# Kernel optimization log

Measured on AMD Instinct MI355X. Metric: run time of the kernel, lower is better.

Reference implementation:

```python
import jax, jax.numpy as jnp
import numpy as np

VEC_DIM = 32
RANK = 2
D = H = W = 40


def setup_inputs() -> dict:
    key = jax.random.key(0)
    k1, k2, k3 = jax.random.split(key, 3)
    volume = jax.random.normal(k1, (D, H, W, VEC_DIM), dtype=jnp.float32)
    # M is nn.Linear(m, m, bias=False) init uniform(-0.5, 0.5)
    M_weight = jax.random.uniform(k2, (VEC_DIM, VEC_DIM), jnp.float32, -0.5, 0.5)
    # P init uniform(-0.1, 0.1)
    P = jax.random.uniform(k3, (VEC_DIM, VEC_DIM), jnp.float32, -0.1, 0.1)
    return {"volume": volume, "M_weight": M_weight, "P": P}


def reference(volume, M_weight, P):
    m = volume.shape[-1]
    r = RANK
    # --- extract_windows: linear mode (step=1), rank_mode='drop', rank_op='avg' ---
    # mean over each r x r x r cubic window == sum-pool / r^3 (VALID padding = drop)
    pooled = jax.lax.reduce_window(
        volume, 0.0, jax.lax.add,
        window_dimensions=(r, r, r, 1),
        window_strides=(1, 1, 1, 1),
        padding="VALID",
    ) / float(r ** 3)  # [Dp, Hp, Wp, m]
    Dp, Hp, Wp = pooled.shape[:3]
    vecs = pooled.reshape(-1, m)  # [B, m], B = Dp*Hp*Wp (window order: k1 outer, k3 inner)
    k1 = jnp.arange(Dp, dtype=jnp.float32)
    k2 = jnp.arange(Hp, dtype=jnp.float32)
    k3 = jnp.arange(Wp, dtype=jnp.float32)
    k1g, k2g, k3g = jnp.meshgrid(k1, k2, k3, indexing="ij")
    k1f, k2f, k3f = k1g.ravel(), k2g.ravel(), k3g.ravel()  # [B]
    # --- batch_compute_Nk ---
    # periods[i, j] = i*m + j + 2
    periods = (jnp.arange(m, dtype=jnp.float32)[:, None] * m
               + jnp.arange(m, dtype=jnp.float32)[None, :] + 2.0)  # [m, m]
    two_pi = 2.0 * jnp.pi
    inv_p = two_pi / periods  # [m, m]
    # phi[b, i, j] = cos(2pi*k1/p) * cos(2pi*k2/p) * cos(2pi*k3/p)
    phi = (jnp.cos(k1f[:, None, None] * inv_p)
           * jnp.cos(k2f[:, None, None] * inv_p)
           * jnp.cos(k3f[:, None, None] * inv_p))  # [B, m, m]
    x = vecs @ M_weight.T  # nn.Linear: x = v W^T, [B, m]
    Nk = jnp.einsum("bj,ij,bij->bi", x, P, phi)  # [B, m]
    return Nk
```

## Files before the change

### kernel.cpp

```cpp
#include <hip/hip_runtime.h>
#include <math.h>

constexpr int DV = 40;
constexpr int NP = 39;
constexpr int VD = 32;
constexpr float TWO_PI = 6.28318530717958647692f;

__global__ __launch_bounds__(256) void ndk_kernel(
    const float* __restrict__ vol,
    const float* __restrict__ Mw,
    const float* __restrict__ P,
    float* __restrict__ out)
{
    __shared__ float  Mt[VD * VD];
    __shared__ float2 RI[VD * VD];
    __shared__ float  pool[8 * VD];
    __shared__ float  xs[NP * VD];

    const int tid = threadIdx.x;
    const int bx  = blockIdx.x;
    const int k1  = bx / NP;
    const int k2  = bx % NP;
    const float k1f = (float)k1, k2f = (float)k2;

    for (int t = tid; t < VD * VD; t += 256) {
        const int row = t >> 5;
        const int col = t & 31;
        Mt[col * VD + row] = Mw[t];
        const float w = TWO_PI / (float)(row * VD + col + 2);
        const float r = P[t] * __cosf(k1f * w) * __cosf(k2f * w);
        RI[col * VD + row] = make_float2(r, w);
    }
    __syncthreads();

    {
        const int c = tid & 31;
        const int s = tid >> 5;
        for (int chunk = 0; chunk < 5; ++chunk) {
            const int k3 = chunk * 8 + s;
            float pv = 0.f;
            if (k3 < NP) {
                const float* vp = vol + ((size_t)(k1 * DV + k2) * DV + k3) * VD + c;
                constexpr int SW = VD;
                constexpr int SH = DV * VD;
                constexpr int SD = DV * DV * VD;
                pv = vp[0]       + vp[SW]
                   + vp[SH]      + vp[SH + SW]
                   + vp[SD]      + vp[SD + SW]
                   + vp[SD + SH] + vp[SD + SH + SW];
                pv *= 0.125f;
            }
            pool[s * VD + c] = pv;
            __syncthreads();
            if (k3 < NP) {
                const int j = c;
                float x = 0.f;
                #pragma unroll
                for (int cc = 0; cc < VD; ++cc)
                    x += pool[s * VD + cc] * Mt[cc * VD + j];
                xs[k3 * VD + j] = x;
            }
            __syncthreads();
        }
    }

    {
        const int i   = tid & 31;
        const int sub = tid >> 5;
        const long bbase = (long)bx * NP;
        for (int k3 = sub; k3 < NP; k3 += 8) {
            const float k3f = (float)k3;
            float acc = 0.f;
            #pragma unroll
            for (int j = 0; j < VD; ++j) {
                const float2 ri = RI[j * VD + i];
                acc += xs[k3 * VD + j] * ri.x * __cosf(k3f * ri.y);
            }
            out[(bbase + k3) * VD + i] = acc;
        }
    }
}

extern "C" void kernel_launch(void* const* d_in, const int* in_sizes, int n_in,
                              void* d_out, int out_size, void* d_ws, size_t ws_size,
                              hipStream_t stream) {
    const float* vol = (const float*)d_in[0];
    const float* Mw  = (const float*)d_in[1];
    const float* P   = (const float*)d_in[2];
    float* out = (float*)d_out;
    (void)in_sizes; (void)n_in; (void)out_size; (void)d_ws; (void)ws_size;

    dim3 grid(NP * NP);
    dim3 block(256);
    ndk_kernel<<<grid, block, 0, stream>>>(vol, Mw, P, out);
}
```

Baseline: 84.99 us.

## Keep M, P-derived coefficients and frequencies in registers instead of shared memory

Drops the shared-memory tables for transposed M and the (P·cos·cos, w) pairs. Each lane now loads its M row and P row straight into registers with float4 loads and computes its coefficients per thread. Shared reads of pool and xs become float4 broadcasts, and one block-wide barrier after the table setup goes away. This cuts shared-memory traffic and LDS footprint, at the cost of roughly 96 extra registers per thread, which may lower occupancy or cause spills.

```diff
diff --git a/kernel.cpp b/kernel.cpp
--- a/kernel.cpp
+++ b/kernel.cpp
@@ -12,71 +12,90 @@
     const float* __restrict__ P,
     float* __restrict__ out)
 {
-    __shared__ float  Mt[VD * VD];
-    __shared__ float2 RI[VD * VD];
-    __shared__ float  pool[8 * VD];
-    __shared__ float  xs[NP * VD];
+    __shared__ alignas(16) float pool[8 * VD];
+    __shared__ alignas(16) float xs[NP * VD];
 
-    const int tid = threadIdx.x;
-    const int bx  = blockIdx.x;
-    const int k1  = bx / NP;
-    const int k2  = bx % NP;
+    const int tid  = threadIdx.x;
+    const int lane = tid & 31;
+    const int sub  = tid >> 5;
+    const int bx = blockIdx.x;
+    const int k1 = bx / NP, k2 = bx % NP;
     const float k1f = (float)k1, k2f = (float)k2;
 
-    for (int t = tid; t < VD * VD; t += 256) {
-        const int row = t >> 5;
-        const int col = t & 31;
-        Mt[col * VD + row] = Mw[t];
-        const float w = TWO_PI / (float)(row * VD + col + 2);
-        const float r = P[t] * __cosf(k1f * w) * __cosf(k2f * w);
-        RI[col * VD + row] = make_float2(r, w);
+    float Mr[VD];
+    {
+        const float4* Mrow = (const float4*)(Mw + lane * VD);
+        #pragma unroll
+        for (int c4 = 0; c4 < 8; ++c4) {
+            float4 m = Mrow[c4];
+            Mr[4*c4+0] = m.x; Mr[4*c4+1] = m.y; Mr[4*c4+2] = m.z; Mr[4*c4+3] = m.w;
+        }
+    }
+
+    const float4* poolv = (const float4*)pool;
+    #pragma unroll
+    for (int t = 0; t < 5; ++t) {
+        const int k3 = t * 8 + sub;
+        float pv = 0.f;
+        if (k3 < NP) {
+            const float* vp = vol + ((size_t)(k1 * DV + k2) * DV + k3) * VD + lane;
+            constexpr int SW = VD, SH = DV * VD, SD = DV * DV * VD;
+            pv = vp[0]       + vp[SW]
+               + vp[SH]      + vp[SH + SW]
+               + vp[SD]      + vp[SD + SW]
+               + vp[SD + SH] + vp[SD + SH + SW];
+            pv *= 0.125f;
+        }
+        __syncthreads();
+        pool[sub * VD + lane] = pv;
+        __syncthreads();
+        if (k3 < NP) {
+            float x = 0.f;
+            #pragma unroll
+            for (int c4 = 0; c4 < 8; ++c4) {
+                float4 p4 = poolv[sub * 8 + c4];
+                x += p4.x * Mr[4*c4+0] + p4.y * Mr[4*c4+1]
+                   + p4.z * Mr[4*c4+2] + p4.w * Mr[4*c4+3];
+            }
+            xs[k3 * VD + lane] = x;
+        }
     }
     __syncthreads();
 
+    float rx[VD], wv[VD];
     {
-        const int c = tid & 31;
-        const int s = tid >> 5;
-        for (int chunk = 0; chunk < 5; ++chunk) {
-            const int k3 = chunk * 8 + s;
-            float pv = 0.f;
-            if (k3 < NP) {
-                const float* vp = vol + ((size_t)(k1 * DV + k2) * DV + k3) * VD + c;
-                constexpr int SW = VD;
-                constexpr int SH = DV * VD;
-                constexpr int SD = DV * DV * VD;
-                pv = vp[0]       + vp[SW]
-                   + vp[SH]      + vp[SH + SW]
-                   + vp[SD]      + vp[SD + SW]
-                   + vp[SD + SH] + vp[SD + SH + SW];
-                pv *= 0.125f;
+        const float4* Prow = (const float4*)(P + lane * VD);
+        #pragma unroll
+        for (int j4 = 0; j4 < 8; ++j4) {
+            float4 p4 = Prow[j4];
+            float pj[4] = { p4.x, p4.y, p4.z, p4.w };
+            #pragma unroll
+            for (int u = 0; u < 4; ++u) {
+                const int j = 4 * j4 + u;
+                const float w = TWO_PI / (float)(lane * VD + j + 2);
+                wv[j] = w;
+                rx[j] = pj[u] * __cosf(k1f * w) * __cosf(k2f * w);
             }
-            pool[s * VD + c] = pv;
-            __syncthreads();
-            if (k3 < NP) {
-                const int j = c;
-                float x = 0.f;
-                #pragma unroll
-                for (int cc = 0; cc < VD; ++cc)
-                    x += pool[s * VD + cc] * Mt[cc * VD + j];
-                xs[k3 * VD + j] = x;
-            }
-            __syncthreads();
         }
     }
 
-    {
-        const int i   = tid & 31;
-        const int sub = tid >> 5;
-        const long bbase = (long)bx * NP;
-        for (int k3 = sub; k3 < NP; k3 += 8) {
+    const float4* xsv = (const float4*)xs;
+    const long obase = (long)bx * NP;
+    #pragma unroll
+    for (int t = 0; t < 5; ++t) {
+        const int k3 = t * 8 + sub;
+        if (k3 < NP) {
             const float k3f = (float)k3;
             float acc = 0.f;
             #pragma unroll
-            for (int j = 0; j < VD; ++j) {
-                const float2 ri = RI[j * VD + i];
-                acc += xs[k3 * VD + j] * ri.x * __cosf(k3f * ri.y);
+            for (int j4 = 0; j4 < 8; ++j4) {
+                float4 xv = xsv[k3 * 8 + j4];
+                acc += xv.x * rx[4*j4+0] * __cosf(k3f * wv[4*j4+0]);
+                acc += xv.y * rx[4*j4+1] * __cosf(k3f * wv[4*j4+1]);
+                acc += xv.z * rx[4*j4+2] * __cosf(k3f * wv[4*j4+2]);
+                acc += xv.w * rx[4*j4+3] * __cosf(k3f * wv[4*j4+3]);
             }
-            out[(bbase + k3) * VD + i] = acc;
+            out[(obase + k3) * VD + lane] = acc;
         }
     }
 }
```

Result: slower. 89.45 us (+5.2%).
